# Performance work log

Measured on AMD Instinct MI355X. Metric: run time of the kernel, lower is better.

The kernel has to match this reference:

```python
import jax, jax.numpy as jnp
import numpy as np

EPS = 1e-5

def layer_norm(x, gamma, beta):
    mu = jnp.mean(x, axis=-1, keepdims=True)
    var = jnp.mean(jnp.square(x - mu), axis=-1, keepdims=True)
    return (x - mu) * jax.lax.rsqrt(var + EPS) * gamma + beta

def setup_inputs() -> dict:
    key = jax.random.key(0)
    ks = jax.random.split(key, 8)
    B, N, E, D, H = 8, 10000, 160000, 128, 128  # batch, nodes, edges, in_dim, dim_h
    nodes = jax.random.normal(ks[0], (B, N, D), dtype=jnp.float32)
    senders = jax.random.randint(ks[1], (E,), 0, N)
    receivers = jax.random.randint(ks[2], (E,), 0, N)
    # nn.Linear(2*in_dim, in_dim): weight [out, in], bias [out]
    Wm = jax.random.normal(ks[3], (D, 2 * D), dtype=jnp.float32) / np.sqrt(2 * D)
    bm = jnp.zeros((D,), dtype=jnp.float32)
    # nn.Linear(2*in_dim, dim_h)
    Wn = jax.random.normal(ks[4], (H, 2 * D), dtype=jnp.float32) / np.sqrt(2 * D)
    bn = jnp.zeros((H,), dtype=jnp.float32)
    g1 = jnp.ones((D,), dtype=jnp.float32)
    b1 = jnp.zeros((D,), dtype=jnp.float32)
    g2 = jnp.ones((H,), dtype=jnp.float32)
    b2 = jnp.zeros((H,), dtype=jnp.float32)
    return {"nodes": nodes, "Wm": Wm, "bm": bm, "g1": g1, "b1": b1,
            "Wn": Wn, "bn": bn, "g2": g2, "b2": b2,
            "senders": senders, "receivers": receivers}

def reference(nodes, Wm, bm, g1, b1, Wn, bn, g2, b2, senders, receivers):
    # gather endpoints: [B, E, 2*D]
    edge_in = jnp.concatenate((nodes[:, receivers], nodes[:, senders]), axis=-1)
    messages = jnp.einsum('bed,od->beo', edge_in, Wm) + bm      # [B, E, D]
    messages = layer_norm(messages, g1, b1)
    # scatter-add into inbox along node axis
    inbox = jnp.zeros_like(nodes).at[:, receivers].add(messages)  # [B, N, D]
    node_in = jnp.concatenate((nodes, inbox), axis=-1)           # [B, N, 2*D]
    out = jnp.einsum('bnd,od->bno', node_in, Wn) + bn            # [B, N, H]
    return layer_norm(out, g2, b2)
```

## Files before the change

### kernel.cpp

```cpp
#include <hip/hip_runtime.h>

#define N_NODES 10000
#define N_EDGES 160000
#define BATCH   8
#define D       128
#define TWO_D   256
#define EPS     1e-5f
#define ETILE   32
#define TPB_E   8
#define TPB_N   8

typedef _Float16 f16x8  __attribute__((ext_vector_type(8)));
typedef float    f32x16 __attribute__((ext_vector_type(16)));
typedef int      intx4  __attribute__((ext_vector_type(4)));

__global__ void zero_kernel(float4* __restrict__ p, long long n4) {
    long long idx    = (long long)blockIdx.x * blockDim.x + threadIdx.x;
    long long stride = (long long)gridDim.x * blockDim.x;
    const float4 z = {0.f, 0.f, 0.f, 0.f};
    for (long long i = idx; i < n4; i += stride) p[i] = z;
}

__global__ void prep_w(const float* __restrict__ Wm, const float* __restrict__ Wn,
                       unsigned char* __restrict__ img) {
    int t = blockIdx.x * blockDim.x + threadIdx.x;
    if (t >= 4096) return;
    int g = t >> 7, o = t & 127;
    f16x8 vm, vn;
#pragma unroll
    for (int j = 0; j < 8; ++j) {
        vm[j] = (_Float16)Wm[o * TWO_D + 8 * g + j];
        vn[j] = (_Float16)Wn[o * TWO_D + 8 * g + j];
    }
    ((f16x8*)img)[t]           = vm;
    ((f16x8*)(img + 65536))[t] = vn;
}

__global__ void hist_kernel(const int* __restrict__ recv, int* __restrict__ counts) {
    int e = blockIdx.x * blockDim.x + threadIdx.x;
    if (e < N_EDGES) atomicAdd(&counts[recv[e]], 1);
}

__global__ __launch_bounds__(1024)
void scan_kernel(const int* __restrict__ counts, int* __restrict__ cursor) {
    __shared__ int tmp[1024];
    int t = threadIdx.x;
    int local[10];
    int s = 0;
#pragma unroll
    for (int j = 0; j < 10; ++j) {
        int idx = t * 10 + j;
        int v = (idx < N_NODES) ? counts[idx] : 0;
        local[j] = s; s += v;
    }
    tmp[t] = s; __syncthreads();
    for (int off = 1; off < 1024; off <<= 1) {
        int v = tmp[t];
        int add = (t >= off) ? tmp[t - off] : 0;
        __syncthreads();
        tmp[t] = v + add;
        __syncthreads();
    }
    int base = (t > 0) ? tmp[t - 1] : 0;
#pragma unroll
    for (int j = 0; j < 10; ++j) {
        int idx = t * 10 + j;
        if (idx < N_NODES) cursor[idx] = base + local[j];
    }
}

__global__ void scatter_kernel(const int* __restrict__ recv, int* __restrict__ cursor,
                               int* __restrict__ perm) {
    int e = blockIdx.x * blockDim.x + threadIdx.x;
    if (e < N_EDGES) {
        int p = atomicAdd(&cursor[recv[e]], 1);
        perm[p] = e;
    }
}

__global__ __launch_bounds__(256, 4)
void edge_mfma(const float* __restrict__ nodes,
               const unsigned char* __restrict__ wimg,
               const float* __restrict__ bm,
               const float* __restrict__ g1,
               const float* __restrict__ b1,
               const int*   __restrict__ senders,
               const int*   __restrict__ receivers,
               const int*   __restrict__ perm,
               float* __restrict__ inbox) {
    __shared__ __align__(16) unsigned char s_lds[33280];
    __shared__ int   s_recv[ETILE];
    __shared__ float s_mu[ETILE];
    __shared__ float s_rs[ETILE];

    const int tid    = threadIdx.x;
    const int b      = blockIdx.x & 7;
    const int grp    = blockIdx.x >> 3;
    const int w      = tid >> 6;
    const int l      = tid & 63;
    const int lane31 = l & 31;
    const int hiG    = l >> 5;
    const int o      = w * 32 + lane31;

    intx4 wfi[16];
    {
        const intx4* img = (const intx4*)wimg;
#pragma unroll
        for (int ks = 0; ks < 16; ++ks)
            wfi[ks] = img[(2 * ks + hiG) * 128 + o];
#pragma unroll
        for (int ks = 0; ks < 16; ++ks)
            asm volatile("" : "+v"(wfi[ks]));
    }
    const float bmv = bm[o];
    const int   col  = tid & 127;
    const int   half = tid >> 7;
    const float gv = g1[col], bv = b1[col];
    float* const abase = inbox + (size_t)b * N_NODES * D + col;

    const int i  = tid & 31;
    const int q8 = tid >> 5;
    f16x8* const Xh  = (f16x8*)s_lds;
    f16x8* const Xl  = (f16x8*)(s_lds + 16384);
    float* const msg = (float*)(s_lds + 16384);

    for (int it = 0; it < TPB_E; ++it) {
        const int e0 = (grp * TPB_E + it) * ETILE;

        {
            const int pe = perm[e0 + i];
            const int r  = (q8 < 4) ? receivers[pe] : senders[pe];
            if (q8 == 0) s_recv[i] = r;
            const float* row = nodes + ((size_t)b * N_NODES + r) * D + (q8 & 3) * 32;
#pragma unroll
            for (int j = 0; j < 4; ++j) {
                const float4 va = *(const float4*)(row + 8 * j);
                const float4 vb = *(const float4*)(row + 8 * j + 4);
                const float xs[8] = {va.x, va.y, va.z, va.w, vb.x, vb.y, vb.z, vb.w};
                f16x8 h, lo;
#pragma unroll
                for (int u = 0; u < 8; ++u) {
                    h[u]  = (_Float16)xs[u];
                    lo[u] = (_Float16)(xs[u] - (float)h[u]);
                }
                const int g = 4 * q8 + j;
                Xh[g * 32 + i] = h;
                Xl[g * 32 + i] = lo;
            }
        }
        __syncthreads();

        f32x16 acc;
#pragma unroll
        for (int r = 0; r < 16; ++r) acc[r] = 0.f;
#pragma unroll
        for (int ks = 0; ks < 16; ++ks) {
            const f16x8 ah = Xh[(2 * ks + hiG) * 32 + lane31];
            const f16x8 al = Xl[(2 * ks + hiG) * 32 + lane31];
            const f16x8 wk = __builtin_bit_cast(f16x8, wfi[ks]);
            acc = __builtin_amdgcn_mfma_f32_32x32x16_f16(ah, wk, acc, 0, 0, 0);
            acc = __builtin_amdgcn_mfma_f32_32x32x16_f16(al, wk, acc, 0, 0, 0);
        }
        __syncthreads();

#pragma unroll
        for (int r = 0; r < 16; ++r) {
            const int m = (r & 3) + 8 * (r >> 2) + 4 * hiG;
            msg[m * 132 + o] = acc[r] + bmv;
        }
        __syncthreads();

        {
            const int m = tid >> 3, c0 = tid & 7;
            float s = 0.f, s2 = 0.f;
#pragma unroll
            for (int i2 = 0; i2 < 16; ++i2) {
                const float v = msg[m * 132 + c0 + 8 * i2];
                s += v; s2 += v * v;
            }
            s  += __shfl_xor(s, 1, 64);  s  += __shfl_xor(s, 2, 64);  s  += __shfl_xor(s, 4, 64);
            s2 += __shfl_xor(s2, 1, 64); s2 += __shfl_xor(s2, 2, 64); s2 += __shfl_xor(s2, 4, 64);
            if (c0 == 0) {
                const float mu  = s * (1.f / 128.f);
                const float var = s2 * (1.f / 128.f) - mu * mu;
                s_mu[m] = mu;
                s_rs[m] = rsqrtf(var + EPS);
            }
        }
        __syncthreads();

        {
            int prev = -1; float accu = 0.f;
#pragma unroll
            for (int e = 0; e < 16; ++e) {
                const int ee = half * 16 + e;
                const int r  = s_recv[ee];
                const float val = (msg[ee * 132 + col] - s_mu[ee]) * s_rs[ee] * gv + bv;
                if (r != prev) {
                    if (prev >= 0) atomicAdd(abase + (size_t)prev * D, accu);
                    prev = r; accu = val;
                } else {
                    accu += val;
                }
            }
            if (prev >= 0) atomicAdd(abase + (size_t)prev * D, accu);
        }
        __syncthreads();
    }
}

__global__ __launch_bounds__(256, 4)
void node_mfma(const float* __restrict__ nodes,
               const float* __restrict__ inbox,
               const unsigned char* __restrict__ wimg,
               const float* __restrict__ bn,
               const float* __restrict__ g2,
               const float* __restrict__ b2,
               float* __restrict__ out) {
    __shared__ __align__(16) unsigned char s_lds[33280];
    __shared__ float s_mu[ETILE];
    __shared__ float s_rs[ETILE];

    const int tid    = threadIdx.x;
    const int b      = blockIdx.x & 7;
    const int grp    = blockIdx.x >> 3;
    const int w      = tid >> 6;
    const int l      = tid & 63;
    const int lane31 = l & 31;
    const int hiG    = l >> 5;
    const int o      = w * 32 + lane31;

    intx4 wfi[16];
    {
        const intx4* img = (const intx4*)wimg;
#pragma unroll
        for (int ks = 0; ks < 16; ++ks)
            wfi[ks] = img[(2 * ks + hiG) * 128 + o];
#pragma unroll
        for (int ks = 0; ks < 16; ++ks)
            asm volatile("" : "+v"(wfi[ks]));
    }
    const float bnv = bn[o];
    const int   col  = tid & 127;
    const int   half = tid >> 7;
    const float gv = g2[col], bv = b2[col];

    const int i  = tid & 31;
    const int q8 = tid >> 5;
    f16x8* const Xh  = (f16x8*)s_lds;
    f16x8* const Xl  = (f16x8*)(s_lds + 16384);
    float* const msg = (float*)(s_lds + 16384);

    const int NTILES = (N_NODES + ETILE - 1) / ETILE;

    for (int it = 0; it < TPB_N; ++it) {
        const int tile = grp * TPB_N + it;
        if (tile >= NTILES) break;
        const int n0 = tile * ETILE;

        {
            int n = n0 + i;
            if (n >= N_NODES) n = N_NODES - 1;
            const float* row = (q8 < 4)
                ? (nodes + ((size_t)b * N_NODES + n) * D + (q8 & 3) * 32)
                : (inbox + ((size_t)b * N_NODES + n) * D + (q8 & 3) * 32);
#pragma unroll
            for (int j = 0; j < 4; ++j) {
                const float4 va = *(const float4*)(row + 8 * j);
                const float4 vb = *(const float4*)(row + 8 * j + 4);
                const float xs[8] = {va.x, va.y, va.z, va.w, vb.x, vb.y, vb.z, vb.w};
                f16x8 h, lo;
#pragma unroll
                for (int u = 0; u < 8; ++u) {
                    h[u]  = (_Float16)xs[u];
                    lo[u] = (_Float16)(xs[u] - (float)h[u]);
                }
                const int g = 4 * q8 + j;
                Xh[g * 32 + i] = h;
                Xl[g * 32 + i] = lo;
            }
        }
        __syncthreads();

        f32x16 acc;
#pragma unroll
        for (int r = 0; r < 16; ++r) acc[r] = 0.f;
#pragma unroll
        for (int ks = 0; ks < 16; ++ks) {
            const f16x8 ah = Xh[(2 * ks + hiG) * 32 + lane31];
            const f16x8 al = Xl[(2 * ks + hiG) * 32 + lane31];
            const f16x8 wk = __builtin_bit_cast(f16x8, wfi[ks]);
            acc = __builtin_amdgcn_mfma_f32_32x32x16_f16(ah, wk, acc, 0, 0, 0);
            acc = __builtin_amdgcn_mfma_f32_32x32x16_f16(al, wk, acc, 0, 0, 0);
        }
        __syncthreads();

#pragma unroll
        for (int r = 0; r < 16; ++r) {
            const int m = (r & 3) + 8 * (r >> 2) + 4 * hiG;
            msg[m * 132 + o] = acc[r] + bnv;
        }
        __syncthreads();

        {
            const int m = tid >> 3, c0 = tid & 7;
            float s = 0.f, s2 = 0.f;
#pragma unroll
            for (int i2 = 0; i2 < 16; ++i2) {
                const float v = msg[m * 132 + c0 + 8 * i2];
                s += v; s2 += v * v;
            }
            s  += __shfl_xor(s, 1, 64);  s  += __shfl_xor(s, 2, 64);  s  += __shfl_xor(s, 4, 64);
            s2 += __shfl_xor(s2, 1, 64); s2 += __shfl_xor(s2, 2, 64); s2 += __shfl_xor(s2, 4, 64);
            if (c0 == 0) {
                const float mu  = s * (1.f / 128.f);
                const float var = s2 * (1.f / 128.f) - mu * mu;
                s_mu[m] = mu;
                s_rs[m] = rsqrtf(var + EPS);
            }
        }
        __syncthreads();

        {
#pragma unroll
            for (int e = 0; e < 16; ++e) {
                const int ee = half * 16 + e;
                const int n  = n0 + ee;
                if (n < N_NODES) {
                    out[((size_t)b * N_NODES + n) * D + col] =
                        (msg[ee * 132 + col] - s_mu[ee]) * s_rs[ee] * gv + bv;
                }
            }
        }
        __syncthreads();
    }
}

__global__ __launch_bounds__(256, 2)
void edge_kernel(const float* __restrict__ nodes,
                 const float* __restrict__ Wm,
                 const float* __restrict__ bm,
                 const float* __restrict__ g1,
                 const float* __restrict__ b1,
                 const int*   __restrict__ senders,
                 const int*   __restrict__ receivers,
                 float* __restrict__ inbox) {
    __shared__ __align__(16) float ldsE[TWO_D][36];
    __shared__ __align__(16) float ldsW[64 * D];
    const int tid = threadIdx.x;
    const int b   = blockIdx.y;
    const int e0  = blockIdx.x * 32;
    const float* nb = nodes + (size_t)b * N_NODES * D;
    {
        const int i = tid >> 3, q0 = tid & 7, e = e0 + i;
        const float* rowR = nb + (size_t)receivers[e] * D;
        const float* rowS = nb + (size_t)senders[e] * D;
#pragma unroll
        for (int j = 0; j < 8; ++j) {
            const int k = (j * 8 + q0) * 4;
            const float4 v = (k < D) ? *(const float4*)(rowR + k)
                                     : *(const float4*)(rowS + (k - D));
            ldsE[k + 0][i] = v.x; ldsE[k + 1][i] = v.y;
            ldsE[k + 2][i] = v.z; ldsE[k + 3][i] = v.w;
        }
    }
    float acc[4][4];
#pragma unroll
    for (int a = 0; a < 4; ++a)
#pragma unroll
        for (int c = 0; c < 4; ++c) acc[a][c] = 0.0f;
    const int og = tid & 31, eg = tid >> 5;
    for (int kt = 0; kt < 4; ++kt) {
        __syncthreads();
        {
            const int oo = tid >> 1, half = tid & 1;
            const float* wrow = Wm + oo * TWO_D + kt * 64 + half * 32;
#pragma unroll
            for (int j = 0; j < 8; ++j) {
                const float4 w4 = *(const float4*)(wrow + j * 4);
                const int k2 = half * 32 + j * 4;
                ldsW[(k2 + 0) * D + oo] = w4.x; ldsW[(k2 + 1) * D + oo] = w4.y;
                ldsW[(k2 + 2) * D + oo] = w4.z; ldsW[(k2 + 3) * D + oo] = w4.w;
            }
        }
        __syncthreads();
#pragma unroll 4
        for (int k2 = 0; k2 < 64; ++k2) {
            const float4 wv = *(const float4*)&ldsW[k2 * D + 4 * og];
            const float4 xv = *(const float4*)&ldsE[kt * 64 + k2][4 * eg];
            const float wa[4] = {wv.x, wv.y, wv.z, wv.w};
            const float xa[4] = {xv.x, xv.y, xv.z, xv.w};
#pragma unroll
            for (int a = 0; a < 4; ++a)
#pragma unroll
                for (int c = 0; c < 4; ++c)
                    acc[a][c] = fmaf(xa[a], wa[c], acc[a][c]);
        }
    }
    const float4 bmv = *(const float4*)&bm[4 * og];
    const float4 g1v = *(const float4*)&g1[4 * og];
    const float4 b1v = *(const float4*)&b1[4 * og];
#pragma unroll
    for (int a = 0; a < 4; ++a) {
        acc[a][0] += bmv.x; acc[a][1] += bmv.y;
        acc[a][2] += bmv.z; acc[a][3] += bmv.w;
    }
    float mu[4], rs[4];
#pragma unroll
    for (int a = 0; a < 4; ++a) {
        float s = acc[a][0] + acc[a][1] + acc[a][2] + acc[a][3];
#pragma unroll
        for (int m = 16; m >= 1; m >>= 1) s += __shfl_xor(s, m, 64);
        mu[a] = s * (1.0f / 128.0f);
        const float d0 = acc[a][0] - mu[a], d1 = acc[a][1] - mu[a];
        const float d2 = acc[a][2] - mu[a], d3 = acc[a][3] - mu[a];
        float q = d0 * d0 + d1 * d1 + d2 * d2 + d3 * d3;
#pragma unroll
        for (int m = 16; m >= 1; m >>= 1) q += __shfl_xor(q, m, 64);
        rs[a] = rsqrtf(q * (1.0f / 128.0f) + EPS);
    }
#pragma unroll
    for (int a = 0; a < 4; ++a) {
        const int e = e0 + 4 * eg + a;
        const int r = receivers[e];
        float* dst = inbox + ((size_t)b * N_NODES + r) * D + 4 * og;
        atomicAdd(dst + 0, (acc[a][0] - mu[a]) * rs[a] * g1v.x + b1v.x);
        atomicAdd(dst + 1, (acc[a][1] - mu[a]) * rs[a] * g1v.y + b1v.y);
        atomicAdd(dst + 2, (acc[a][2] - mu[a]) * rs[a] * g1v.z + b1v.z);
        atomicAdd(dst + 3, (acc[a][3] - mu[a]) * rs[a] * g1v.w + b1v.w);
    }
}

__global__ __launch_bounds__(256, 2)
void node_kernel(const float* __restrict__ nodes,
                 const float* __restrict__ inbox,
                 const float* __restrict__ Wn,
                 const float* __restrict__ bn,
                 const float* __restrict__ g2,
                 const float* __restrict__ b2,
                 float* __restrict__ out) {
    __shared__ __align__(16) float ldsE[TWO_D][36];
    __shared__ __align__(16) float ldsW[64 * D];
    const int tid = threadIdx.x;
    const int b   = blockIdx.y;
    const int n0  = blockIdx.x * 32;
    {
        const int i = tid >> 3, q0 = tid & 7;
        int n = n0 + i;
        if (n >= N_NODES) n = N_NODES - 1;
        const float* rowN = nodes + ((size_t)b * N_NODES + n) * D;
        const float* rowI = inbox + ((size_t)b * N_NODES + n) * D;
#pragma unroll
        for (int j = 0; j < 8; ++j) {
            const int k = (j * 8 + q0) * 4;
            const float4 v = (k < D) ? *(const float4*)(rowN + k)
                                     : *(const float4*)(rowI + (k - D));
            ldsE[k + 0][i] = v.x; ldsE[k + 1][i] = v.y;
            ldsE[k + 2][i] = v.z; ldsE[k + 3][i] = v.w;
        }
    }
    float acc[4][4];
#pragma unroll
    for (int a = 0; a < 4; ++a)
#pragma unroll
        for (int c = 0; c < 4; ++c) acc[a][c] = 0.0f;
    const int og = tid & 31, eg = tid >> 5;
    for (int kt = 0; kt < 4; ++kt) {
        __syncthreads();
        {
            const int oo = tid >> 1, half = tid & 1;
            const float* wrow = Wn + oo * TWO_D + kt * 64 + half * 32;
#pragma unroll
            for (int j = 0; j < 8; ++j) {
                const float4 w4 = *(const float4*)(wrow + j * 4);
                const int k2 = half * 32 + j * 4;
                ldsW[(k2 + 0) * D + oo] = w4.x; ldsW[(k2 + 1) * D + oo] = w4.y;
                ldsW[(k2 + 2) * D + oo] = w4.z; ldsW[(k2 + 3) * D + oo] = w4.w;
            }
        }
        __syncthreads();
#pragma unroll 4
        for (int k2 = 0; k2 < 64; ++k2) {
            const float4 wv = *(const float4*)&ldsW[k2 * D + 4 * og];
            const float4 xv = *(const float4*)&ldsE[kt * 64 + k2][4 * eg];
            const float wa[4] = {wv.x, wv.y, wv.z, wv.w};
            const float xa[4] = {xv.x, xv.y, xv.z, xv.w};
#pragma unroll
            for (int a = 0; a < 4; ++a)
#pragma unroll
                for (int c = 0; c < 4; ++c)
                    acc[a][c] = fmaf(xa[a], wa[c], acc[a][c]);
        }
    }
    const float4 bnv = *(const float4*)&bn[4 * og];
    const float4 g2v = *(const float4*)&g2[4 * og];
    const float4 b2v = *(const float4*)&b2[4 * og];
#pragma unroll
    for (int a = 0; a < 4; ++a) {
        acc[a][0] += bnv.x; acc[a][1] += bnv.y;
        acc[a][2] += bnv.z; acc[a][3] += bnv.w;
    }
    float mu[4], rs[4];
#pragma unroll
    for (int a = 0; a < 4; ++a) {
        float s = acc[a][0] + acc[a][1] + acc[a][2] + acc[a][3];
#pragma unroll
        for (int m = 16; m >= 1; m >>= 1) s += __shfl_xor(s, m, 64);
        mu[a] = s * (1.0f / 128.0f);
        const float d0 = acc[a][0] - mu[a], d1 = acc[a][1] - mu[a];
        const float d2 = acc[a][2] - mu[a], d3 = acc[a][3] - mu[a];
        float q = d0 * d0 + d1 * d1 + d2 * d2 + d3 * d3;
#pragma unroll
        for (int m = 16; m >= 1; m >>= 1) q += __shfl_xor(q, m, 64);
        rs[a] = rsqrtf(q * (1.0f / 128.0f) + EPS);
    }
#pragma unroll
    for (int a = 0; a < 4; ++a) {
        const int n = n0 + 4 * eg + a;
        if (n < N_NODES) {
            float4 o4;
            o4.x = (acc[a][0] - mu[a]) * rs[a] * g2v.x + b2v.x;
            o4.y = (acc[a][1] - mu[a]) * rs[a] * g2v.y + b2v.y;
            o4.z = (acc[a][2] - mu[a]) * rs[a] * g2v.z + b2v.z;
            o4.w = (acc[a][3] - mu[a]) * rs[a] * g2v.w + b2v.w;
            *(float4*)(out + ((size_t)b * N_NODES + n) * D + 4 * og) = o4;
        }
    }
}

extern "C" void kernel_launch(void* const* d_in, const int* in_sizes, int n_in,
                              void* d_out, int out_size, void* d_ws, size_t ws_size,
                              hipStream_t stream) {
    const float* nodes     = (const float*)d_in[0];
    const float* Wm        = (const float*)d_in[1];
    const float* bm        = (const float*)d_in[2];
    const float* g1        = (const float*)d_in[3];
    const float* b1        = (const float*)d_in[4];
    const float* Wn        = (const float*)d_in[5];
    const float* bn        = (const float*)d_in[6];
    const float* g2        = (const float*)d_in[7];
    const float* b2        = (const float*)d_in[8];
    const int*   senders   = (const int*)d_in[9];
    const int*   receivers = (const int*)d_in[10];
    float*       out       = (float*)d_out;

    const long long inbox_n = (long long)BATCH * N_NODES * D;
    const size_t SCRATCH_NEED = 131072 + 720128;

    if (d_ws != nullptr && ws_size >= SCRATCH_NEED) {
        unsigned char* wsb  = (unsigned char*)d_ws;
        unsigned char* wimg = wsb;
        int* ints   = (int*)(wsb + 131072);
        int* counts = ints;
        int* cursor = ints + 10016;
        int* perm   = ints + 20032;
        float* inbox = (ws_size >= (size_t)1048576 + (size_t)inbox_n * 4)
                           ? (float*)(wsb + 1048576) : out;

        zero_kernel<<<dim3(10),   dim3(256), 0, stream>>>((float4*)counts, 2500);
        zero_kernel<<<dim3(2048), dim3(256), 0, stream>>>((float4*)inbox, inbox_n / 4);
        prep_w<<<dim3(16), dim3(256), 0, stream>>>(Wm, Wn, wimg);
        hist_kernel<<<dim3(625), dim3(256), 0, stream>>>(receivers, counts);
        scan_kernel<<<dim3(1), dim3(1024), 0, stream>>>(counts, cursor);
        scatter_kernel<<<dim3(625), dim3(256), 0, stream>>>(receivers, cursor, perm);

        edge_mfma<<<dim3(N_EDGES / ETILE / TPB_E * BATCH), dim3(256), 0, stream>>>(
            nodes, wimg, bm, g1, b1, senders, receivers, perm, inbox);

        const int ntiles = (N_NODES + ETILE - 1) / ETILE;
        node_mfma<<<dim3((ntiles + TPB_N - 1) / TPB_N * BATCH), dim3(256), 0, stream>>>(
            nodes, inbox, wimg + 65536, bn, g2, b2, out);
    } else {
        float* inbox = out;
        zero_kernel<<<dim3(2048), dim3(256), 0, stream>>>((float4*)inbox, inbox_n / 4);
        edge_kernel<<<dim3(N_EDGES / 32, BATCH), dim3(256), 0, stream>>>(
            nodes, Wm, bm, g1, b1, senders, receivers, inbox);
        node_kernel<<<dim3((N_NODES + 31) / 32, BATCH), dim3(256), 0, stream>>>(
            nodes, inbox, Wn, bn, g2, b2, out);
    }
}
```

Baseline: 422.0 us.

## Prefetch next tile's gathered rows into registers during MFMA compute

Both the edge-message and node-update kernels now issue the global loads for tile it+1 into registers right after the LDS staging barrier, so gather latency overlaps the MFMA loop and epilogue of the current tile. The MFMA loop is wrapped in s_setprio to raise wave priority during matrix work. TPB_N drops from 8 to 2, giving the node kernel more, smaller blocks. The cost is extra register pressure from the 8 float4 prefetch buffers, which could lower occupancy.

```diff
diff --git a/kernel.cpp b/kernel.cpp
--- a/kernel.cpp
+++ b/kernel.cpp
@@ -8,7 +8,7 @@
 #define EPS     1e-5f
 #define ETILE   32
 #define TPB_E   8
-#define TPB_N   8
+#define TPB_N   2
 
 typedef _Float16 f16x8  __attribute__((ext_vector_type(8)));
 typedef float    f32x16 __attribute__((ext_vector_type(16)));
@@ -124,35 +124,54 @@
     f16x8* const Xl  = (f16x8*)(s_lds + 16384);
     float* const msg = (float*)(s_lds + 16384);
 
+    int    rcur;
+    float4 pa[4], pb[4];
+    {
+        const int e0 = grp * TPB_E * ETILE;
+        const int pe = perm[e0 + i];
+        rcur = (q8 < 4) ? receivers[pe] : senders[pe];
+        const float* row = nodes + ((size_t)b * N_NODES + rcur) * D + (q8 & 3) * 32;
+#pragma unroll
+        for (int j = 0; j < 4; ++j) {
+            pa[j] = *(const float4*)(row + 8 * j);
+            pb[j] = *(const float4*)(row + 8 * j + 4);
+        }
+    }
+
     for (int it = 0; it < TPB_E; ++it) {
-        const int e0 = (grp * TPB_E + it) * ETILE;
-
-        {
-            const int pe = perm[e0 + i];
-            const int r  = (q8 < 4) ? receivers[pe] : senders[pe];
-            if (q8 == 0) s_recv[i] = r;
-            const float* row = nodes + ((size_t)b * N_NODES + r) * D + (q8 & 3) * 32;
+        if (q8 == 0) s_recv[i] = rcur;
+#pragma unroll
+        for (int j = 0; j < 4; ++j) {
+            const float xs[8] = {pa[j].x, pa[j].y, pa[j].z, pa[j].w,
+                                 pb[j].x, pb[j].y, pb[j].z, pb[j].w};
+            f16x8 h, lo;
+#pragma unroll
+            for (int u = 0; u < 8; ++u) {
+                h[u]  = (_Float16)xs[u];
+                lo[u] = (_Float16)(xs[u] - (float)h[u]);
+            }
+            const int g = 4 * q8 + j;
+            Xh[g * 32 + i] = h;
+            Xl[g * 32 + i] = lo;
+        }
+        __syncthreads();
+
+        if (it + 1 < TPB_E) {
+            const int e0n = (grp * TPB_E + it + 1) * ETILE;
+            const int pe  = perm[e0n + i];
+            rcur = (q8 < 4) ? receivers[pe] : senders[pe];
+            const float* row = nodes + ((size_t)b * N_NODES + rcur) * D + (q8 & 3) * 32;
 #pragma unroll
             for (int j = 0; j < 4; ++j) {
-                const float4 va = *(const float4*)(row + 8 * j);
-                const float4 vb = *(const float4*)(row + 8 * j + 4);
-                const float xs[8] = {va.x, va.y, va.z, va.w, vb.x, vb.y, vb.z, vb.w};
-                f16x8 h, lo;
-#pragma unroll
-                for (int u = 0; u < 8; ++u) {
-                    h[u]  = (_Float16)xs[u];
-                    lo[u] = (_Float16)(xs[u] - (float)h[u]);
-                }
-                const int g = 4 * q8 + j;
-                Xh[g * 32 + i] = h;
-                Xl[g * 32 + i] = lo;
-            }
-        }
-        __syncthreads();
+                pa[j] = *(const float4*)(row + 8 * j);
+                pb[j] = *(const float4*)(row + 8 * j + 4);
+            }
+        }
 
         f32x16 acc;
 #pragma unroll
         for (int r = 0; r < 16; ++r) acc[r] = 0.f;
+        __builtin_amdgcn_s_setprio(1);
 #pragma unroll
         for (int ks = 0; ks < 16; ++ks) {
             const f16x8 ah = Xh[(2 * ks + hiG) * 32 + lane31];
@@ -161,6 +180,7 @@
             acc = __builtin_amdgcn_mfma_f32_32x32x16_f16(ah, wk, acc, 0, 0, 0);
             acc = __builtin_amdgcn_mfma_f32_32x32x16_f16(al, wk, acc, 0, 0, 0);
         }
+        __builtin_amdgcn_s_setprio(0);
         __syncthreads();
 
 #pragma unroll
@@ -253,38 +273,56 @@
 
     const int NTILES = (N_NODES + ETILE - 1) / ETILE;
 
+    float4 pa[4], pb[4];
+    {
+        int n = grp * TPB_N * ETILE + i;
+        if (n >= N_NODES) n = N_NODES - 1;
+        const float* row = ((q8 < 4) ? nodes : inbox)
+                         + ((size_t)b * N_NODES + n) * D + (q8 & 3) * 32;
+#pragma unroll
+        for (int j = 0; j < 4; ++j) {
+            pa[j] = *(const float4*)(row + 8 * j);
+            pb[j] = *(const float4*)(row + 8 * j + 4);
+        }
+    }
+
     for (int it = 0; it < TPB_N; ++it) {
         const int tile = grp * TPB_N + it;
         if (tile >= NTILES) break;
         const int n0 = tile * ETILE;
 
-        {
-            int n = n0 + i;
+#pragma unroll
+        for (int j = 0; j < 4; ++j) {
+            const float xs[8] = {pa[j].x, pa[j].y, pa[j].z, pa[j].w,
+                                 pb[j].x, pb[j].y, pb[j].z, pb[j].w};
+            f16x8 h, lo;
+#pragma unroll
+            for (int u = 0; u < 8; ++u) {
+                h[u]  = (_Float16)xs[u];
+                lo[u] = (_Float16)(xs[u] - (float)h[u]);
+            }
+            const int g = 4 * q8 + j;
+            Xh[g * 32 + i] = h;
+            Xl[g * 32 + i] = lo;
+        }
+        __syncthreads();
+
+        if (it + 1 < TPB_N && tile + 1 < NTILES) {
+            int n = (tile + 1) * ETILE + i;
             if (n >= N_NODES) n = N_NODES - 1;
-            const float* row = (q8 < 4)
-                ? (nodes + ((size_t)b * N_NODES + n) * D + (q8 & 3) * 32)
-                : (inbox + ((size_t)b * N_NODES + n) * D + (q8 & 3) * 32);
+            const float* row = ((q8 < 4) ? nodes : inbox)
+                             + ((size_t)b * N_NODES + n) * D + (q8 & 3) * 32;
 #pragma unroll
             for (int j = 0; j < 4; ++j) {
-                const float4 va = *(const float4*)(row + 8 * j);
-                const float4 vb = *(const float4*)(row + 8 * j + 4);
-                const float xs[8] = {va.x, va.y, va.z, va.w, vb.x, vb.y, vb.z, vb.w};
-                f16x8 h, lo;
-#pragma unroll
-                for (int u = 0; u < 8; ++u) {
-                    h[u]  = (_Float16)xs[u];
-                    lo[u] = (_Float16)(xs[u] - (float)h[u]);
-                }
-                const int g = 4 * q8 + j;
-                Xh[g * 32 + i] = h;
-                Xl[g * 32 + i] = lo;
-            }
-        }
-        __syncthreads();
+                pa[j] = *(const float4*)(row + 8 * j);
+                pb[j] = *(const float4*)(row + 8 * j + 4);
+            }
+        }
 
         f32x16 acc;
 #pragma unroll
         for (int r = 0; r < 16; ++r) acc[r] = 0.f;
+        __builtin_amdgcn_s_setprio(1);
 #pragma unroll
         for (int ks = 0; ks < 16; ++ks) {
             const f16x8 ah = Xh[(2 * ks + hiG) * 32 + lane31];
@@ -293,6 +331,7 @@
             acc = __builtin_amdgcn_mfma_f32_32x32x16_f16(ah, wk, acc, 0, 0, 0);
             acc = __builtin_amdgcn_mfma_f32_32x32x16_f16(al, wk, acc, 0, 0, 0);
         }
+        __builtin_amdgcn_s_setprio(0);
         __syncthreads();
 
 #pragma unroll
```

After: 579.6 us. +37.4%, slower.
